# Performance work log

Measured on AMD Instinct MI355X. Metric: run time of the kernel, lower is better.

The kernel has to match this reference:

```python
import jax, jax.numpy as jnp
import numpy as np

B, T, D_IN, D_STATE, N_NEURONS, D_OUT = 256, 512, 128, 128, 2048, 64


def setup_inputs() -> dict:
    key = jax.random.key(0)
    ks = jax.random.split(key, 6)
    d_aug = D_IN + D_STATE
    seq = jax.random.normal(ks[0], (B, T, D_IN), dtype=jnp.float32)
    # hypersphere-style encoders: unit-norm rows over the augmented input space
    enc = jax.random.normal(ks[1], (N_NEURONS, d_aug), dtype=jnp.float32)
    encoders = enc / jnp.linalg.norm(enc, axis=1, keepdims=True)
    gain = jax.random.uniform(ks[2], (N_NEURONS,), minval=0.5, maxval=2.0, dtype=jnp.float32)
    bias = jax.random.normal(ks[3], (N_NEURONS,), dtype=jnp.float32)
    # decoders are analytically fit in the original; use small random values so the
    # recurrent feedback path carries nontrivial signal
    state_decoders = jax.random.normal(ks[4], (N_NEURONS, D_STATE), dtype=jnp.float32) * 0.02
    decoders = jax.random.normal(ks[5], (N_NEURONS, D_OUT), dtype=jnp.float32) * 0.02
    return {"seq": seq, "encoders": encoders, "gain": gain, "bias": bias,
            "state_decoders": state_decoders, "decoders": decoders}


def reference(seq, encoders, gain, bias, state_decoders, decoders):
    # seq: (B, T, d_in); encoders: (N, d_in+d_state); state_decoders: (N, d_state)
    b = seq.shape[0]
    d_state = state_decoders.shape[1]
    n = encoders.shape[0]
    seq_t = jnp.swapaxes(seq, 0, 1)  # (T, B, d_in)

    def step(carry, u):
        s, _ = carry  # s: (B, d_state)
        x_aug = jnp.concatenate([u, s], axis=-1)          # (B, d_in+d_state)
        a = jax.nn.relu(gain * (x_aug @ encoders.T) + bias)  # (B, N)
        return (a @ state_decoders, a), None

    init = (jnp.zeros((b, d_state), seq.dtype), jnp.zeros((b, n), seq.dtype))
    (_, a_final), _ = jax.lax.scan(step, init, seq_t)
    return a_final @ decoders  # (B, d_out)
```

## Files before the change

kernel.cpp:

```cpp
#include <hip/hip_runtime.h>


constexpr int CB   = 256;
constexpr int CT   = 512;
constexpr int DIN  = 128;
constexpr int DST  = 128;
constexpr int DOUT = 64;
constexpr int DAUG = 256;

constexpr int NBG = 16;
constexpr int NNG = 8;
constexpr int BT  = 16;
constexpr int NT  = 256;

constexpr int EPAD = 264;
constexpr int APAD = 264;

using f32x4  = __attribute__((ext_vector_type(4))) float;
using bf16x8 = __attribute__((ext_vector_type(8))) short;

__device__ __forceinline__ short f2b(float x) {
  unsigned u = __builtin_bit_cast(unsigned, x);
  u += 0x7fffu + ((u >> 16) & 1u);
  return (short)(u >> 16);
}
__device__ __forceinline__ short4 f2b4(float4 v) {
  return make_short4(f2b(v.x), f2b(v.y), f2b(v.z), f2b(v.w));
}

__global__ void nef_init(float* Sbuf, unsigned int* ctrs, float* out) {
  int idx = blockIdx.x * blockDim.x + threadIdx.x;
  int stride = gridDim.x * blockDim.x;
  for (int i = idx; i < 4 * CB * DST; i += stride) Sbuf[i] = 0.f;
  for (int i = idx; i < CB * DOUT; i += stride) out[i] = 0.f;
  if (idx < 16 * 64) ctrs[idx] = 0u;
}

__global__ void __launch_bounds__(256) nef_main(
    const float* __restrict__ seq,  const float* __restrict__ enc,
    const float* __restrict__ gainp,const float* __restrict__ biasp,
    const float* __restrict__ sdec, const float* __restrict__ dec,
    float* __restrict__ out, float* __restrict__ Sbuf, unsigned int* ctrs)
{
  __shared__ short E_lds[NT][EPAD];
  __shared__ short X_lds[BT][EPAD];
  __shared__ short A_lds[BT][APAD];
  __shared__ float gain_lds[NT];
  __shared__ float bias_lds[NT];

  const int tid  = threadIdx.x;
  const int bg   = blockIdx.x & 15;
  const int ng   = blockIdx.x >> 4;
  const int b0   = bg * BT;
  const int n0   = ng * NT;
  const int wave = tid >> 6;
  const int lane = tid & 63;
  const int l15  = lane & 15;
  const int lhi  = lane >> 4;
  const int kbase = lhi * 8;

  for (int i = 0; i < 64; ++i) {
    int fidx = i * 256 + tid;
    int row = fidx >> 6, c4 = fidx & 63;
    const float4 v = *(const float4*)(enc + (size_t)(n0 + row) * DAUG + (c4 << 2));
    *(short4*)&E_lds[row][c4 << 2] = f2b4(v);
  }
  if (tid < NT) { gain_lds[tid] = gainp[n0 + tid]; bias_lds[tid] = biasp[n0 + tid]; }
  else if (tid < 2 * NT) {  }
  if (tid >= NT) { gain_lds[tid & 255] = gain_lds[tid & 255]; }

  bf16x8 sdt0[8], sdt1[8];
#pragma unroll
  for (int kk = 0; kk < 8; ++kk) {
    bf16x8 f0, f1;
    const int dA = wave * 32 + l15, dB = dA + 16;
#pragma unroll
    for (int j = 0; j < 8; ++j) {
      const size_t nrow = (size_t)(n0 + kk * 32 + kbase + j) * DST;
      f0[j] = f2b(sdec[nrow + dA]);
      f1[j] = f2b(sdec[nrow + dB]);
    }
    sdt0[kk] = f0; sdt1[kk] = f1;
  }

  unsigned int* ctr = ctrs + bg * 64;
  const int nsub = wave * 64;

  float4 pu[2];
#pragma unroll
  for (int i = 0; i < 2; ++i) {
    int fidx = i * 256 + tid;
    int row = fidx >> 5, c4 = fidx & 31;
    pu[i] = *(const float4*)(seq + ((size_t)(b0 + row) * CT + 0) * DIN + (c4 << 2));
  }
#pragma unroll
  for (int i = 0; i < 2; ++i) {
    int fidx = i * 256 + tid;
    int row = fidx >> 5, c4 = fidx & 31;
    *(short4*)&X_lds[row][c4 << 2] = f2b4(pu[i]);
    pu[i] = *(const float4*)(seq + ((size_t)(b0 + row) * CT + 1) * DIN + (c4 << 2));
  }
  __syncthreads();

  for (int t = 0; t < CT; ++t) {
    {
      float* Sz = Sbuf + ((t + 2) & 3) * (CB * DST);
      __hip_atomic_store(&Sz[b0 * DST + ng * 256 + tid], 0.f,
                         __ATOMIC_RELAXED, __HIP_MEMORY_SCOPE_AGENT);
    }

    f32x4 acc0 = {0,0,0,0}, acc1 = {0,0,0,0}, acc2 = {0,0,0,0}, acc3 = {0,0,0,0};
#pragma unroll
    for (int kk = 0; kk < 4; ++kk) {
      bf16x8 a = *(const bf16x8*)&X_lds[l15][kk * 32 + kbase];
      bf16x8 e0 = *(const bf16x8*)&E_lds[nsub +      l15][kk * 32 + kbase];
      bf16x8 e1 = *(const bf16x8*)&E_lds[nsub + 16 + l15][kk * 32 + kbase];
      bf16x8 e2 = *(const bf16x8*)&E_lds[nsub + 32 + l15][kk * 32 + kbase];
      bf16x8 e3 = *(const bf16x8*)&E_lds[nsub + 48 + l15][kk * 32 + kbase];
      acc0 = __builtin_amdgcn_mfma_f32_16x16x32_bf16(a, e0, acc0, 0, 0, 0);
      acc1 = __builtin_amdgcn_mfma_f32_16x16x32_bf16(a, e1, acc1, 0, 0, 0);
      acc2 = __builtin_amdgcn_mfma_f32_16x16x32_bf16(a, e2, acc2, 0, 0, 0);
      acc3 = __builtin_amdgcn_mfma_f32_16x16x32_bf16(a, e3, acc3, 0, 0, 0);
    }

    if (t > 0) {
      unsigned int tgt = 8u * (unsigned)t, guard = 0;
      while (__hip_atomic_load(ctr, __ATOMIC_RELAXED, __HIP_MEMORY_SCOPE_AGENT) < tgt) {
        __builtin_amdgcn_s_sleep(1);
        if (++guard > 100000u) break;
      }
    }
    {
      const float* Sr = Sbuf + (t & 3) * (CB * DST);
      int row = tid >> 4, c8 = tid & 15;
      const unsigned long long* p =
          (const unsigned long long*)(Sr + (size_t)(b0 + row) * DST + c8 * 8);
      short s8[8];
#pragma unroll
      for (int q = 0; q < 4; ++q) {
        unsigned long long w = __hip_atomic_load(p + q, __ATOMIC_RELAXED,
                                                 __HIP_MEMORY_SCOPE_AGENT);
        s8[2 * q]     = f2b(__builtin_bit_cast(float, (unsigned)(w & 0xffffffffu)));
        s8[2 * q + 1] = f2b(__builtin_bit_cast(float, (unsigned)(w >> 32)));
      }
      *(short4*)&X_lds[row][DIN + c8 * 8]     = make_short4(s8[0], s8[1], s8[2], s8[3]);
      *(short4*)&X_lds[row][DIN + c8 * 8 + 4] = make_short4(s8[4], s8[5], s8[6], s8[7]);
    }
    __syncthreads();

#pragma unroll
    for (int kk = 4; kk < 8; ++kk) {
      bf16x8 a = *(const bf16x8*)&X_lds[l15][kk * 32 + kbase];
      bf16x8 e0 = *(const bf16x8*)&E_lds[nsub +      l15][kk * 32 + kbase];
      bf16x8 e1 = *(const bf16x8*)&E_lds[nsub + 16 + l15][kk * 32 + kbase];
      bf16x8 e2 = *(const bf16x8*)&E_lds[nsub + 32 + l15][kk * 32 + kbase];
      bf16x8 e3 = *(const bf16x8*)&E_lds[nsub + 48 + l15][kk * 32 + kbase];
      acc0 = __builtin_amdgcn_mfma_f32_16x16x32_bf16(a, e0, acc0, 0, 0, 0);
      acc1 = __builtin_amdgcn_mfma_f32_16x16x32_bf16(a, e1, acc1, 0, 0, 0);
      acc2 = __builtin_amdgcn_mfma_f32_16x16x32_bf16(a, e2, acc2, 0, 0, 0);
      acc3 = __builtin_amdgcn_mfma_f32_16x16x32_bf16(a, e3, acc3, 0, 0, 0);
    }
    {
      const int nc0 = nsub + l15, nc1 = nc0 + 16, nc2 = nc0 + 32, nc3 = nc0 + 48;
      const float g0 = gain_lds[nc0], bi0 = bias_lds[nc0];
      const float g1 = gain_lds[nc1], bi1 = bias_lds[nc1];
      const float g2 = gain_lds[nc2], bi2 = bias_lds[nc2];
      const float g3 = gain_lds[nc3], bi3 = bias_lds[nc3];
#pragma unroll
      for (int j = 0; j < 4; ++j) {
        A_lds[lhi * 4 + j][nc0] = f2b(fmaxf(g0 * acc0[j] + bi0, 0.f));
        A_lds[lhi * 4 + j][nc1] = f2b(fmaxf(g1 * acc1[j] + bi1, 0.f));
        A_lds[lhi * 4 + j][nc2] = f2b(fmaxf(g2 * acc2[j] + bi2, 0.f));
        A_lds[lhi * 4 + j][nc3] = f2b(fmaxf(g3 * acc3[j] + bi3, 0.f));
      }
    }
    __syncthreads();

    if (t != CT - 1) {
      f32x4 p0 = {0,0,0,0}, p1 = {0,0,0,0};
#pragma unroll
      for (int kk = 0; kk < 8; ++kk) {
        bf16x8 a = *(const bf16x8*)&A_lds[l15][kk * 32 + kbase];
        p0 = __builtin_amdgcn_mfma_f32_16x16x32_bf16(a, sdt0[kk], p0, 0, 0, 0);
        p1 = __builtin_amdgcn_mfma_f32_16x16x32_bf16(a, sdt1[kk], p1, 0, 0, 0);
      }
      float* Sw = Sbuf + ((t + 1) & 3) * (CB * DST);
      const int dA = wave * 32 + l15, dB = dA + 16;
#pragma unroll
      for (int j = 0; j < 4; ++j) {
        unsafeAtomicAdd(&Sw[(size_t)(b0 + lhi * 4 + j) * DST + dA], p0[j]);
        unsafeAtomicAdd(&Sw[(size_t)(b0 + lhi * 4 + j) * DST + dB], p1[j]);
      }
#pragma unroll
      for (int i = 0; i < 2; ++i) {
        int fidx = i * 256 + tid;
        int row = fidx >> 5, c4 = fidx & 31;
        *(short4*)&X_lds[row][c4 << 2] = f2b4(pu[i]);
      }
      __syncthreads();
      if (tid == 0) atomicAdd(ctr, 1u);
      if (t + 2 < CT) {
#pragma unroll
        for (int i = 0; i < 2; ++i) {
          int fidx = i * 256 + tid;
          int row = fidx >> 5, c4 = fidx & 31;
          pu[i] = *(const float4*)(seq + ((size_t)(b0 + row) * CT + (t + 2)) * DIN + (c4 << 2));
        }
      }
    } else {
      f32x4 o0 = {0,0,0,0};
      const int ocol = wave * 16 + l15;
#pragma unroll
      for (int kk = 0; kk < 8; ++kk) {
        bf16x8 a = *(const bf16x8*)&A_lds[l15][kk * 32 + kbase];
        bf16x8 bfD;
#pragma unroll
        for (int j = 0; j < 8; ++j)
          bfD[j] = f2b(dec[(size_t)(n0 + kk * 32 + kbase + j) * DOUT + ocol]);
        o0 = __builtin_amdgcn_mfma_f32_16x16x32_bf16(a, bfD, o0, 0, 0, 0);
      }
#pragma unroll
      for (int j = 0; j < 4; ++j)
        unsafeAtomicAdd(&out[(size_t)(b0 + lhi * 4 + j) * DOUT + ocol], o0[j]);
    }
  }
}

extern "C" void kernel_launch(void* const* d_in, const int* in_sizes, int n_in,
                              void* d_out, int out_size, void* d_ws, size_t ws_size,
                              hipStream_t stream) {
  const float* seq   = (const float*)d_in[0];
  const float* enc   = (const float*)d_in[1];
  const float* gainp = (const float*)d_in[2];
  const float* biasp = (const float*)d_in[3];
  const float* sdec  = (const float*)d_in[4];
  const float* dec   = (const float*)d_in[5];
  float* out = (float*)d_out;

  float* Sbuf = (float*)d_ws;
  unsigned int* ctrs = (unsigned int*)((char*)d_ws + (size_t)4 * CB * DST * sizeof(float));

  nef_init<<<128, 256, 0, stream>>>(Sbuf, ctrs, out);
  nef_main<<<dim3(NBG * NNG), dim3(256), 0, stream>>>(seq, enc, gainp, biasp,
                                                      sdec, dec, out, Sbuf, ctrs);
}
```

Measured before the change: 1.505 ms.

## Replace atomic-add state reduction with per-block partial slots and step flags

Result: slower. 2.165 ms (+43.8%).

```diff
diff --git a/kernel.cpp b/kernel.cpp
--- a/kernel.cpp
+++ b/kernel.cpp
@@ -28,19 +28,22 @@
   return make_short4(f2b(v.x), f2b(v.y), f2b(v.z), f2b(v.w));
 }
 
-__global__ void nef_init(float* Sbuf, unsigned int* ctrs, float* out) {
+constexpr size_t PBUF_ELEMS  = (size_t)2 * NBG * NNG * BT * DST;
+constexpr int    SLOT        = BT * DST;
+
+__global__ void nef_init(float* Pbuf, unsigned int* Pflag, float* out) {
   int idx = blockIdx.x * blockDim.x + threadIdx.x;
   int stride = gridDim.x * blockDim.x;
-  for (int i = idx; i < 4 * CB * DST; i += stride) Sbuf[i] = 0.f;
+  for (int i = idx; i < 2 * NBG * 64; i += stride) Pflag[i] = 0u;
   for (int i = idx; i < CB * DOUT; i += stride) out[i] = 0.f;
-  if (idx < 16 * 64) ctrs[idx] = 0u;
+  (void)Pbuf;
 }
 
 __global__ void __launch_bounds__(256) nef_main(
     const float* __restrict__ seq,  const float* __restrict__ enc,
     const float* __restrict__ gainp,const float* __restrict__ biasp,
     const float* __restrict__ sdec, const float* __restrict__ dec,
-    float* __restrict__ out, float* __restrict__ Sbuf, unsigned int* ctrs)
+    float* __restrict__ out, float* __restrict__ Pbuf, unsigned int* Pflag)
 {
   __shared__ short E_lds[NT][EPAD];
   __shared__ short X_lds[BT][EPAD];
@@ -65,9 +68,8 @@
     const float4 v = *(const float4*)(enc + (size_t)(n0 + row) * DAUG + (c4 << 2));
     *(short4*)&E_lds[row][c4 << 2] = f2b4(v);
   }
-  if (tid < NT) { gain_lds[tid] = gainp[n0 + tid]; bias_lds[tid] = biasp[n0 + tid]; }
-  else if (tid < 2 * NT) {  }
-  if (tid >= NT) { gain_lds[tid & 255] = gain_lds[tid & 255]; }
+  gain_lds[tid] = gainp[n0 + tid];
+  bias_lds[tid] = biasp[n0 + tid];
 
   bf16x8 sdt0[8], sdt1[8];
 #pragma unroll
@@ -83,7 +85,6 @@
     sdt0[kk] = f0; sdt1[kk] = f1;
   }
 
-  unsigned int* ctr = ctrs + bg * 64;
   const int nsub = wave * 64;
 
   float4 pu[2];
@@ -103,12 +104,6 @@
   __syncthreads();
 
   for (int t = 0; t < CT; ++t) {
-    {
-      float* Sz = Sbuf + ((t + 2) & 3) * (CB * DST);
-      __hip_atomic_store(&Sz[b0 * DST + ng * 256 + tid], 0.f,
-                         __ATOMIC_RELAXED, __HIP_MEMORY_SCOPE_AGENT);
-    }
-
     f32x4 acc0 = {0,0,0,0}, acc1 = {0,0,0,0}, acc2 = {0,0,0,0}, acc3 = {0,0,0,0};
 #pragma unroll
     for (int kk = 0; kk < 4; ++kk) {
@@ -123,28 +118,45 @@
       acc3 = __builtin_amdgcn_mfma_f32_16x16x32_bf16(a, e3, acc3, 0, 0, 0);
     }
 
-    if (t > 0) {
-      unsigned int tgt = 8u * (unsigned)t, guard = 0;
-      while (__hip_atomic_load(ctr, __ATOMIC_RELAXED, __HIP_MEMORY_SCOPE_AGENT) < tgt) {
-        __builtin_amdgcn_s_sleep(1);
-        if (++guard > 100000u) break;
-      }
-    }
-    {
-      const float* Sr = Sbuf + (t & 3) * (CB * DST);
+    if (t == 0) {
       int row = tid >> 4, c8 = tid & 15;
-      const unsigned long long* p =
-          (const unsigned long long*)(Sr + (size_t)(b0 + row) * DST + c8 * 8);
-      short s8[8];
-#pragma unroll
-      for (int q = 0; q < 4; ++q) {
-        unsigned long long w = __hip_atomic_load(p + q, __ATOMIC_RELAXED,
-                                                 __HIP_MEMORY_SCOPE_AGENT);
-        s8[2 * q]     = f2b(__builtin_bit_cast(float, (unsigned)(w & 0xffffffffu)));
-        s8[2 * q + 1] = f2b(__builtin_bit_cast(float, (unsigned)(w >> 32)));
-      }
-      *(short4*)&X_lds[row][DIN + c8 * 8]     = make_short4(s8[0], s8[1], s8[2], s8[3]);
-      *(short4*)&X_lds[row][DIN + c8 * 8 + 4] = make_short4(s8[4], s8[5], s8[6], s8[7]);
+      *(short4*)&X_lds[row][DIN + c8 * 8]     = make_short4(0, 0, 0, 0);
+      *(short4*)&X_lds[row][DIN + c8 * 8 + 4] = make_short4(0, 0, 0, 0);
+    } else {
+      {
+        const unsigned int* fl = Pflag + ((size_t)(t & 1) * NBG + bg) * 64;
+        unsigned int guard = 0;
+        for (;;) {
+          unsigned v = (lane < NNG)
+              ? __hip_atomic_load(&fl[lane], __ATOMIC_RELAXED, __HIP_MEMORY_SCOPE_AGENT)
+              : (unsigned)t;
+          if (__all(v == (unsigned)t)) break;
+          __builtin_amdgcn_s_sleep(1);
+          if (++guard > 100000u) break;
+        }
+      }
+      const float* Pb = Pbuf + ((size_t)(t & 1) * NBG + bg) * (NNG * SLOT);
+      int row = tid >> 4, c8 = tid & 15;
+      float r0=0,r1=0,r2=0,r3=0,r4=0,r5=0,r6=0,r7=0;
+#pragma unroll
+      for (int s = 0; s < NNG; ++s) {
+        const unsigned long long* p =
+            (const unsigned long long*)(Pb + (size_t)s * SLOT + row * DST + c8 * 8);
+        unsigned long long w0 = __hip_atomic_load(p + 0, __ATOMIC_RELAXED, __HIP_MEMORY_SCOPE_AGENT);
+        unsigned long long w1 = __hip_atomic_load(p + 1, __ATOMIC_RELAXED, __HIP_MEMORY_SCOPE_AGENT);
+        unsigned long long w2 = __hip_atomic_load(p + 2, __ATOMIC_RELAXED, __HIP_MEMORY_SCOPE_AGENT);
+        unsigned long long w3 = __hip_atomic_load(p + 3, __ATOMIC_RELAXED, __HIP_MEMORY_SCOPE_AGENT);
+        r0 += __builtin_bit_cast(float, (unsigned)(w0 & 0xffffffffu));
+        r1 += __builtin_bit_cast(float, (unsigned)(w0 >> 32));
+        r2 += __builtin_bit_cast(float, (unsigned)(w1 & 0xffffffffu));
+        r3 += __builtin_bit_cast(float, (unsigned)(w1 >> 32));
+        r4 += __builtin_bit_cast(float, (unsigned)(w2 & 0xffffffffu));
+        r5 += __builtin_bit_cast(float, (unsigned)(w2 >> 32));
+        r6 += __builtin_bit_cast(float, (unsigned)(w3 & 0xffffffffu));
+        r7 += __builtin_bit_cast(float, (unsigned)(w3 >> 32));
+      }
+      *(short4*)&X_lds[row][DIN + c8 * 8]     = make_short4(f2b(r0), f2b(r1), f2b(r2), f2b(r3));
+      *(short4*)&X_lds[row][DIN + c8 * 8 + 4] = make_short4(f2b(r4), f2b(r5), f2b(r6), f2b(r7));
     }
     __syncthreads();
 
@@ -184,12 +196,15 @@
         p0 = __builtin_amdgcn_mfma_f32_16x16x32_bf16(a, sdt0[kk], p0, 0, 0, 0);
         p1 = __builtin_amdgcn_mfma_f32_16x16x32_bf16(a, sdt1[kk], p1, 0, 0, 0);
       }
-      float* Sw = Sbuf + ((t + 1) & 3) * (CB * DST);
+      float* Pw = Pbuf + ((size_t)((t + 1) & 1) * NBG + bg) * (NNG * SLOT)
+                       + (size_t)ng * SLOT;
       const int dA = wave * 32 + l15, dB = dA + 16;
 #pragma unroll
       for (int j = 0; j < 4; ++j) {
-        unsafeAtomicAdd(&Sw[(size_t)(b0 + lhi * 4 + j) * DST + dA], p0[j]);
-        unsafeAtomicAdd(&Sw[(size_t)(b0 + lhi * 4 + j) * DST + dB], p1[j]);
+        __hip_atomic_store(&Pw[(lhi * 4 + j) * DST + dA], p0[j],
+                           __ATOMIC_RELAXED, __HIP_MEMORY_SCOPE_AGENT);
+        __hip_atomic_store(&Pw[(lhi * 4 + j) * DST + dB], p1[j],
+                           __ATOMIC_RELAXED, __HIP_MEMORY_SCOPE_AGENT);
       }
 #pragma unroll
       for (int i = 0; i < 2; ++i) {
@@ -198,7 +213,10 @@
         *(short4*)&X_lds[row][c4 << 2] = f2b4(pu[i]);
       }
       __syncthreads();
-      if (tid == 0) atomicAdd(ctr, 1u);
+      if (tid == 0)
+        __hip_atomic_store(&Pflag[((size_t)((t + 1) & 1) * NBG + bg) * 64 + ng],
+                           (unsigned)(t + 1),
+                           __ATOMIC_RELAXED, __HIP_MEMORY_SCOPE_AGENT);
       if (t + 2 < CT) {
 #pragma unroll
         for (int i = 0; i < 2; ++i) {
@@ -237,10 +255,10 @@
   const float* dec   = (const float*)d_in[5];
   float* out = (float*)d_out;
 
-  float* Sbuf = (float*)d_ws;
-  unsigned int* ctrs = (unsigned int*)((char*)d_ws + (size_t)4 * CB * DST * sizeof(float));
-
-  nef_init<<<128, 256, 0, stream>>>(Sbuf, ctrs, out);
+  float* Pbuf = (float*)d_ws;
+  unsigned int* Pflag = (unsigned int*)((char*)d_ws + PBUF_ELEMS * sizeof(float));
+
+  nef_init<<<128, 256, 0, stream>>>(Pbuf, Pflag, out);
   nef_main<<<dim3(NBG * NNG), dim3(256), 0, stream>>>(seq, enc, gainp, biasp,
-                                                      sdec, dec, out, Sbuf, ctrs);
-}
+                                                      sdec, dec, out, Pbuf, Pflag);
+}
```
